# Kernel tuning notes

Hardware: AMD Instinct MI355X
Metric: run time of the kernel (lower is better)

The kernel has to match this reference:

```python
import jax, jax.numpy as jnp
import numpy as np

D_MODEL = 512
N_STATE = 512  # must equal D_MODEL (torch code broadcasts B*(N,) against u[:,t] of (batch,d_model))
BATCH = 8
SEQ_LEN = 4096
DT_MIN, DT_MAX = 0.001, 0.1


def setup_inputs() -> dict:
    key = jax.random.key(0)
    k_u, k_lam, k_b, k_q, k_dt = jax.random.split(key, 5)
    u = jax.random.normal(k_u, (BATCH, SEQ_LEN, D_MODEL), dtype=jnp.float32)
    Lambda = jax.random.normal(k_lam, (N_STATE,), dtype=jnp.float32)
    B = jax.random.normal(k_b, (N_STATE,), dtype=jnp.float32)
    Q = jax.random.normal(k_q, (N_STATE, D_MODEL), dtype=jnp.float32) / np.sqrt(N_STATE)
    log_dt = jax.random.uniform(k_dt, (1,), dtype=jnp.float32) * (np.log(DT_MAX) - np.log(DT_MIN)) + np.log(DT_MIN)
    return {"u": u, "Lambda": Lambda, "B": B, "Q": Q, "log_dt": log_dt}


def reference(u, Lambda, B, Q, log_dt):
    # dt = exp(log_dt); A = diag(exp(dt * -exp(Lambda))) -> x @ A.T == x * a
    dt = jnp.exp(log_dt)              # (1,)
    a = jnp.exp(dt * (-jnp.exp(Lambda)))  # (N,)
    Bdt = dt * B                      # (N,)

    u_t = jnp.transpose(u, (1, 0, 2))  # (L, batch, N)

    def step(x, ut):
        x = x * a + Bdt * ut           # diagonal recurrence, (batch, N)
        return x, x

    x0 = jnp.zeros((u.shape[0], Lambda.shape[0]), dtype=u.dtype)
    _, xs = jax.lax.scan(step, x0, u_t)       # (L, batch, N)
    y = jnp.einsum('lbn,nd->bld', xs, Q)      # project to d_model
    return y
```

## Files before the change

kernel.cpp:

```cpp
#include <hip/hip_runtime.h>
#include <hip/hip_bf16.h>

#define BATCH 8
#define SEQ   4096
#define NST   512
#define DM    512
#define NCHUNK 32
#define TCH    128

typedef __attribute__((ext_vector_type(4))) float f32x4;
typedef __attribute__((ext_vector_type(2))) float f32x2;
typedef __attribute__((ext_vector_type(8))) short short8v;
typedef __attribute__((ext_vector_type(4))) short short4v;

__device__ __forceinline__ short f2bf(float f) {
  union { float f; unsigned u; } v; v.f = f;
  unsigned r = v.u + 0x7FFFu + ((v.u >> 16) & 1u);
  return (short)(r >> 16);
}

__global__ void k_scan_sums(const float* __restrict__ u, const float* __restrict__ Lam,
                            const float* __restrict__ Bv, const float* __restrict__ log_dt,
                            float* __restrict__ S) {
  int gid = blockIdx.x * 256 + threadIdx.x;
  int n2 = (gid & 255) * 2;
  int bc = gid >> 8;
  int b  = bc & (BATCH - 1);
  int c  = bc >> 3;
  float dt = expf(log_dt[0]);
  f32x2 lam = *(const f32x2*)(Lam + n2);
  f32x2 bv  = *(const f32x2*)(Bv + n2);
  float a0 = expf(-dt * expf(lam[0])), a1 = expf(-dt * expf(lam[1]));
  float g0 = dt * bv[0],               g1 = dt * bv[1];
  const float* up = u + ((size_t)b * SEQ + (size_t)c * TCH) * NST + n2;
  float s0 = 0.f, s1 = 0.f;
  #pragma unroll 8
  for (int t = 0; t < TCH; ++t) {
    f32x2 v = *(const f32x2*)(up + (size_t)t * NST);
    s0 = fmaf(a0, s0, g0 * v[0]);
    s1 = fmaf(a1, s1, g1 * v[1]);
  }
  *(f32x2*)(S + (c * BATCH + b) * NST + n2) = (f32x2){s0, s1};
}

__global__ void k_propagate(const float* __restrict__ Lam, const float* __restrict__ log_dt,
                            const float* __restrict__ S, float* __restrict__ Xc) {
  int gid = blockIdx.x * 256 + threadIdx.x;
  int n = gid & (NST - 1);
  int b = gid >> 9;
  float dt = expf(log_dt[0]);
  float a  = expf(-dt * expf(Lam[n]));
  float aT = a;
  #pragma unroll
  for (int i = 0; i < 7; ++i) aT *= aT;
  float x = 0.f;
  for (int c = 0; c < NCHUNK; ++c) {
    Xc[(c * BATCH + b) * NST + n] = x;
    x = fmaf(aT, x, S[(c * BATCH + b) * NST + n]);
  }
}

__global__ void k_transQ(const float* __restrict__ Q, short* __restrict__ Qt) {
  __shared__ short tile[64][68];
  int bn = (blockIdx.x & 7) * 64;
  int bd = (blockIdx.x >> 3) * 64;
  int tc = threadIdx.x & 15;
  int tr = threadIdx.x >> 4;
  #pragma unroll
  for (int i = 0; i < 4; ++i) {
    int r = tr + i * 16;
    f32x4 v = *(const f32x4*)(Q + (size_t)(bn + r) * DM + bd + tc * 4);
    short4v h;
    h[0] = f2bf(v[0]); h[1] = f2bf(v[1]); h[2] = f2bf(v[2]); h[3] = f2bf(v[3]);
    *(short4v*)&tile[r][tc * 4] = h;
  }
  __syncthreads();
  #pragma unroll
  for (int i = 0; i < 4; ++i) {
    int r = tr + i * 16;
    short4v h;
    #pragma unroll
    for (int j = 0; j < 4; ++j) h[j] = tile[tc * 4 + j][r];
    *(short4v*)(Qt + (size_t)(bd + r) * NST + bn + tc * 4) = h;
  }
}

__global__ __launch_bounds__(512, 2) void k_fused(
    const float* __restrict__ u, const float* __restrict__ Lam,
    const float* __restrict__ Bv, const float* __restrict__ log_dt,
    const float* __restrict__ Xc, const short* __restrict__ Qt,
    float* __restrict__ y) {
  __shared__ __align__(16) short X[TCH][NST + 8];
  const int tid = threadIdx.x;
  const int b = blockIdx.x & (BATCH - 1);
  const int c = blockIdx.x >> 3;

  {
    const int n = tid;
    float dt = expf(log_dt[0]);
    float a  = expf(-dt * expf(Lam[n]));
    float g  = dt * Bv[n];
    float x  = Xc[(c * BATCH + b) * NST + n];
    const float* up = u + ((size_t)b * SEQ + (size_t)c * TCH) * NST + n;
    #pragma unroll 8
    for (int t = 0; t < TCH; ++t) {
      x = fmaf(a, x, g * up[(size_t)t * NST]);
      X[t][n] = f2bf(x);
    }
  }
  __syncthreads();

  const int lane = tid & 63;
  const int wid  = tid >> 6;
  const int wr   = wid >> 2;
  const int wc   = wid & 3;
  const int l15  = lane & 15;
  const int lhi  = lane >> 4;
  const int ka   = lhi * 8;

  f32x4 acc[4][8];
  #pragma unroll
  for (int mi = 0; mi < 4; ++mi)
    #pragma unroll
    for (int nf = 0; nf < 8; ++nf) acc[mi][nf] = (f32x4){0.f, 0.f, 0.f, 0.f};

  for (int k0 = 0; k0 < NST; k0 += 32) {
    short8v afrag[4];
    #pragma unroll
    for (int mi = 0; mi < 4; ++mi)
      afrag[mi] = *(const short8v*)&X[wr * 64 + mi * 16 + l15][k0 + ka];
    short8v bfrag[8];
    #pragma unroll
    for (int nf = 0; nf < 8; ++nf)
      bfrag[nf] = *(const short8v*)(Qt + (size_t)(wc * 128 + nf * 16 + l15) * NST + k0 + ka);
    #pragma unroll
    for (int mi = 0; mi < 4; ++mi)
      #pragma unroll
      for (int nf = 0; nf < 8; ++nf)
        acc[mi][nf] = __builtin_amdgcn_mfma_f32_16x16x32_bf16(afrag[mi], bfrag[nf], acc[mi][nf], 0, 0, 0);
  }
  __syncthreads();

  float* Yb = (float*)&X[0][0];
  #pragma unroll
  for (int g = 0; g < 4; ++g) {
    const int gwr = g >> 1, m0 = (g & 1) * 2;
    if (wr == gwr) {
      #pragma unroll
      for (int mm = 0; mm < 2; ++mm) {
        const int mi = m0 + mm;
        #pragma unroll
        for (int nf = 0; nf < 8; ++nf) {
          const int r0 = mm * 16 + lhi * 4;
          const int cc = wc * 128 + nf * 16 + l15;
          #pragma unroll
          for (int i = 0; i < 4; ++i)
            Yb[(r0 + i) * DM + cc] = acc[mi][nf][i];
        }
      }
    }
    __syncthreads();
    const size_t rowbase = (size_t)b * SEQ + (size_t)c * TCH + g * 32;
    #pragma unroll
    for (int j = 0; j < 8; ++j) {
      const int q  = tid + j * 512;
      const int fi = q * 4;
      const int r  = fi >> 9;
      const int col = fi & (DM - 1);
      *(f32x4*)(y + (rowbase + r) * DM + col) = *(const f32x4*)(Yb + fi);
    }
    __syncthreads();
  }
}

extern "C" void kernel_launch(void* const* d_in, const int* in_sizes, int n_in,
                              void* d_out, int out_size, void* d_ws, size_t ws_size,
                              hipStream_t stream) {
  const float* u      = (const float*)d_in[0];
  const float* Lam    = (const float*)d_in[1];
  const float* Bv     = (const float*)d_in[2];
  const float* Q      = (const float*)d_in[3];
  const float* log_dt = (const float*)d_in[4];
  float* out = (float*)d_out;

  float* S  = (float*)d_ws;
  float* Xc = S + NCHUNK * BATCH * NST;
  short* Qt = (short*)(Xc + NCHUNK * BATCH * NST);

  hipLaunchKernelGGL(k_scan_sums, dim3(NCHUNK * BATCH * 256 / 256), dim3(256), 0, stream,
                     u, Lam, Bv, log_dt, S);
  hipLaunchKernelGGL(k_propagate, dim3(BATCH * NST / 256), dim3(256), 0, stream,
                     Lam, log_dt, S, Xc);
  hipLaunchKernelGGL(k_transQ, dim3(64), dim3(256), 0, stream, Q, Qt);
  hipLaunchKernelGGL(k_fused, dim3(NCHUNK * BATCH), dim3(512), 0, stream,
                     u, Lam, Bv, log_dt, Xc, Qt, out);
}
```

Measured before the change: 70.36 us.

## Split fused chunk into two sub-tiles, overlap scan loads with MFMA, store directly

The fused kernel now handles each 128-step chunk as two 64-step halves in double-buffered shared memory. Loads of u for the second half are issued inside the first half's MFMA loop, and the second half's scan runs after the first result is stored. Each wave now owns a 64x64 output tile and writes accumulators straight to global memory, replacing the staged shared-memory transpose and coalesced vector stores. This cuts LDS use and barriers and overlaps scan latency with matrix work, at the cost of more registers (64-float arrays, dropped occupancy hint), Q fragments fetched twice, and scattered scalar global stores.

```diff
diff --git a/kernel.cpp b/kernel.cpp
--- a/kernel.cpp
+++ b/kernel.cpp
@@ -7,6 +7,8 @@
 #define DM    512
 #define NCHUNK 32
 #define TCH    128
+#define ST     64
+#define LDP    (NST + 8)
 
 typedef __attribute__((ext_vector_type(4))) float f32x4;
 typedef __attribute__((ext_vector_type(2))) float f32x2;
@@ -85,92 +87,121 @@
   }
 }
 
-__global__ __launch_bounds__(512, 2) void k_fused(
+__global__ __launch_bounds__(512) void k_fused(
     const float* __restrict__ u, const float* __restrict__ Lam,
     const float* __restrict__ Bv, const float* __restrict__ log_dt,
     const float* __restrict__ Xc, const short* __restrict__ Qt,
     float* __restrict__ y) {
-  __shared__ __align__(16) short X[TCH][NST + 8];
+  __shared__ __align__(16) short X[2][ST][LDP];
   const int tid = threadIdx.x;
   const int b = blockIdx.x & (BATCH - 1);
   const int c = blockIdx.x >> 3;
 
+  const float dt = expf(log_dt[0]);
+  const float a  = expf(-dt * expf(Lam[tid]));
+  const float g  = dt * Bv[tid];
+  float x = Xc[(c * BATCH + b) * NST + tid];
+  const float* up = u + ((size_t)b * SEQ + (size_t)c * TCH) * NST + tid;
+
   {
-    const int n = tid;
-    float dt = expf(log_dt[0]);
-    float a  = expf(-dt * expf(Lam[n]));
-    float g  = dt * Bv[n];
-    float x  = Xc[(c * BATCH + b) * NST + n];
-    const float* up = u + ((size_t)b * SEQ + (size_t)c * TCH) * NST + n;
-    #pragma unroll 8
-    for (int t = 0; t < TCH; ++t) {
-      x = fmaf(a, x, g * up[(size_t)t * NST]);
-      X[t][n] = f2bf(x);
+    float ur[ST];
+    #pragma unroll
+    for (int t = 0; t < ST; ++t) ur[t] = up[(size_t)t * NST];
+    #pragma unroll
+    for (int t = 0; t < ST; ++t) {
+      x = fmaf(a, x, g * ur[t]);
+      X[0][t][tid] = f2bf(x);
     }
   }
   __syncthreads();
 
   const int lane = tid & 63;
-  const int wid  = tid >> 6;
-  const int wr   = wid >> 2;
-  const int wc   = wid & 3;
+  const int wc   = tid >> 6;
   const int l15  = lane & 15;
   const int lhi  = lane >> 4;
   const int ka   = lhi * 8;
-
-  f32x4 acc[4][8];
-  #pragma unroll
-  for (int mi = 0; mi < 4; ++mi)
-    #pragma unroll
-    for (int nf = 0; nf < 8; ++nf) acc[mi][nf] = (f32x4){0.f, 0.f, 0.f, 0.f};
-
-  for (int k0 = 0; k0 < NST; k0 += 32) {
+  const short* qbase = Qt + (size_t)(wc * 64 + l15) * NST + ka;
+  float* yb = y + ((size_t)b * SEQ + (size_t)c * TCH) * DM;
+
+  float ur2[ST];
+  f32x4 acc[4][4];
+  #pragma unroll
+  for (int mi = 0; mi < 4; ++mi)
+    #pragma unroll
+    for (int nf = 0; nf < 4; ++nf) acc[mi][nf] = (f32x4){0.f, 0.f, 0.f, 0.f};
+
+  #pragma unroll
+  for (int kk = 0; kk < 16; ++kk) {
+    const int k0 = kk * 32;
+    #pragma unroll
+    for (int j = 0; j < 4; ++j)
+      ur2[kk * 4 + j] = up[(size_t)(ST + kk * 4 + j) * NST];
     short8v afrag[4];
     #pragma unroll
     for (int mi = 0; mi < 4; ++mi)
-      afrag[mi] = *(const short8v*)&X[wr * 64 + mi * 16 + l15][k0 + ka];
-    short8v bfrag[8];
-    #pragma unroll
-    for (int nf = 0; nf < 8; ++nf)
-      bfrag[nf] = *(const short8v*)(Qt + (size_t)(wc * 128 + nf * 16 + l15) * NST + k0 + ka);
-    #pragma unroll
-    for (int mi = 0; mi < 4; ++mi)
-      #pragma unroll
-      for (int nf = 0; nf < 8; ++nf)
+      afrag[mi] = *(const short8v*)&X[0][mi * 16 + l15][k0 + ka];
+    short8v bfrag[4];
+    #pragma unroll
+    for (int nf = 0; nf < 4; ++nf)
+      bfrag[nf] = *(const short8v*)(qbase + (size_t)nf * 16 * NST + k0);
+    #pragma unroll
+    for (int mi = 0; mi < 4; ++mi)
+      #pragma unroll
+      for (int nf = 0; nf < 4; ++nf)
         acc[mi][nf] = __builtin_amdgcn_mfma_f32_16x16x32_bf16(afrag[mi], bfrag[nf], acc[mi][nf], 0, 0, 0);
   }
+
+  #pragma unroll
+  for (int mi = 0; mi < 4; ++mi)
+    #pragma unroll
+    for (int nf = 0; nf < 4; ++nf) {
+      const int rr = mi * 16 + lhi * 4;
+      const int cc = wc * 64 + nf * 16 + l15;
+      #pragma unroll
+      for (int i = 0; i < 4; ++i)
+        yb[(size_t)(rr + i) * DM + cc] = acc[mi][nf][i];
+    }
+
+  #pragma unroll
+  for (int t = 0; t < ST; ++t) {
+    x = fmaf(a, x, g * ur2[t]);
+    X[1][t][tid] = f2bf(x);
+  }
   __syncthreads();
 
-  float* Yb = (float*)&X[0][0];
-  #pragma unroll
-  for (int g = 0; g < 4; ++g) {
-    const int gwr = g >> 1, m0 = (g & 1) * 2;
-    if (wr == gwr) {
-      #pragma unroll
-      for (int mm = 0; mm < 2; ++mm) {
-        const int mi = m0 + mm;
-        #pragma unroll
-        for (int nf = 0; nf < 8; ++nf) {
-          const int r0 = mm * 16 + lhi * 4;
-          const int cc = wc * 128 + nf * 16 + l15;
-          #pragma unroll
-          for (int i = 0; i < 4; ++i)
-            Yb[(r0 + i) * DM + cc] = acc[mi][nf][i];
-        }
-      }
+  #pragma unroll
+  for (int mi = 0; mi < 4; ++mi)
+    #pragma unroll
+    for (int nf = 0; nf < 4; ++nf) acc[mi][nf] = (f32x4){0.f, 0.f, 0.f, 0.f};
+
+  #pragma unroll
+  for (int kk = 0; kk < 16; ++kk) {
+    const int k0 = kk * 32;
+    short8v afrag[4];
+    #pragma unroll
+    for (int mi = 0; mi < 4; ++mi)
+      afrag[mi] = *(const short8v*)&X[1][mi * 16 + l15][k0 + ka];
+    short8v bfrag[4];
+    #pragma unroll
+    for (int nf = 0; nf < 4; ++nf)
+      bfrag[nf] = *(const short8v*)(qbase + (size_t)nf * 16 * NST + k0);
+    #pragma unroll
+    for (int mi = 0; mi < 4; ++mi)
+      #pragma unroll
+      for (int nf = 0; nf < 4; ++nf)
+        acc[mi][nf] = __builtin_amdgcn_mfma_f32_16x16x32_bf16(afrag[mi], bfrag[nf], acc[mi][nf], 0, 0, 0);
+  }
+
+  #pragma unroll
+  for (int mi = 0; mi < 4; ++mi)
+    #pragma unroll
+    for (int nf = 0; nf < 4; ++nf) {
+      const int rr = ST + mi * 16 + lhi * 4;
+      const int cc = wc * 64 + nf * 16 + l15;
+      #pragma unroll
+      for (int i = 0; i < 4; ++i)
+        yb[(size_t)(rr + i) * DM + cc] = acc[mi][nf][i];
     }
-    __syncthreads();
-    const size_t rowbase = (size_t)b * SEQ + (size_t)c * TCH + g * 32;
-    #pragma unroll
-    for (int j = 0; j < 8; ++j) {
-      const int q  = tid + j * 512;
-      const int fi = q * 4;
-      const int r  = fi >> 9;
-      const int col = fi & (DM - 1);
-      *(f32x4*)(y + (rowbase + r) * DM + col) = *(const f32x4*)(Yb + fi);
-    }
-    __syncthreads();
-  }
 }
 
 extern "C" void kernel_launch(void* const* d_in, const int* in_sizes, int n_in,
@@ -187,7 +218,7 @@
   float* Xc = S + NCHUNK * BATCH * NST;
   short* Qt = (short*)(Xc + NCHUNK * BATCH * NST);
 
-  hipLaunchKernelGGL(k_scan_sums, dim3(NCHUNK * BATCH * 256 / 256), dim3(256), 0, stream,
+  hipLaunchKernelGGL(k_scan_sums, dim3(NCHUNK * BATCH), dim3(256), 0, stream,
                      u, Lam, Bv, log_dt, S);
   hipLaunchKernelGGL(k_propagate, dim3(BATCH * NST / 256), dim3(256), 0, stream,
                      Lam, log_dt, S, Xc);
```

New measurement: 65.55 us. 6.8% less time.
